# Kernel optimization log

Hardware: AMD Instinct MI355X
Metric: run time of the kernel (lower is better)

## Reference

```python
import jax, jax.numpy as jnp
import numpy as np
from jax import lax

NPOINT, RADIUS, NSAMPLE, EPS = 2048, 0.1, 32, 1e-5


def setup_inputs() -> dict:
    key = jax.random.key(0)
    ks = jax.random.split(key, 8)
    B, N, D, CIN, COUT, DEPTH = 4, 8192, 29, 32, 64, 2
    return {
        "xyz": jax.random.uniform(ks[0], (B, 3, N), jnp.float32),
        "points": jax.random.normal(ks[1], (B, D, N), jnp.float32),
        "proj_w": jax.random.normal(ks[2], (COUT, CIN), jnp.float32) * 0.05,
        "proj_g": jnp.ones((COUT,), jnp.float32),
        "proj_b": jnp.zeros((COUT,), jnp.float32),
        "w1": jax.random.normal(ks[3], (DEPTH, COUT, COUT), jnp.float32) * 0.05,
        "g1": jnp.ones((DEPTH, COUT), jnp.float32),
        "b1": jnp.zeros((DEPTH, COUT), jnp.float32),
        "w2": jax.random.normal(ks[4], (DEPTH, COUT, COUT), jnp.float32) * 0.05,
        "g2": jnp.ones((DEPTH, COUT), jnp.float32),
        "b2": jnp.zeros((DEPTH, COUT), jnp.float32),
    }


def fps(xyz, npoint):
    # xyz: [B,N,3] -> idx [B,npoint]; deterministic start at index 0
    B, N, _ = xyz.shape
    def body(carry, _):
        dist, far = carry  # [B,N], [B]
        centroid = jnp.take_along_axis(xyz, far[:, None, None], axis=1)  # [B,1,3]
        d = jnp.sum((xyz - centroid) ** 2, -1)
        dist = jnp.minimum(dist, d)
        return (dist, jnp.argmax(dist, -1).astype(jnp.int32)), far
    init = (jnp.full((B, N), 1e10, xyz.dtype), jnp.zeros((B,), jnp.int32))
    _, idx = lax.scan(body, init, None, length=npoint)
    return jnp.transpose(idx)  # [B,npoint]


def ball_query(radius, nsample, xyz, new_xyz):
    # matches torch query_ball_point: invalid -> N, sort, take first nsample, backfill
    N = xyz.shape[1]
    sqr = (jnp.sum(new_xyz ** 2, -1)[:, :, None]
           + jnp.sum(xyz ** 2, -1)[:, None, :]
           - 2.0 * jnp.einsum("bsc,bnc->bsn", new_xyz, xyz))  # [B,S,N]
    cand = jnp.where(sqr <= radius * radius, jnp.arange(N, dtype=jnp.int32), jnp.int32(N))
    neg, _ = lax.top_k(-cand, nsample)
    idx = -neg  # nsample smallest indices, ascending
    first = idx[:, :, :1]
    return jnp.where(idx == N, first, idx)  # [B,S,K]


def gather_nb(p, idx):
    # p [B,N,C], idx [B,S,K] -> [B,S,K,C]
    return jax.vmap(lambda pb, ib: pb[ib])(p, idx)


def _conv(x, w):
    # 1x1 conv: w [O,C], x [B,C,K,S]
    return jnp.einsum("oc,bcks->boks", w, x)


def _bn(x, g, b):
    # training-mode BatchNorm2d over (B,K,S) per channel
    m = jnp.mean(x, (0, 2, 3), keepdims=True)
    v = jnp.var(x, (0, 2, 3), keepdims=True)
    return g[None, :, None, None] * (x - m) * lax.rsqrt(v + EPS) + b[None, :, None, None]


def reference(xyz, points, proj_w, proj_g, proj_b, w1, g1, b1, w2, g2, b2):
    xyz_t = jnp.transpose(xyz, (0, 2, 1))      # [B,N,3]
    pts_t = jnp.transpose(points, (0, 2, 1))   # [B,N,D]
    fidx = fps(xyz_t, NPOINT)                  # [B,S]
    new_xyz = jnp.take_along_axis(xyz_t, fidx[:, :, None], axis=1)  # [B,S,3]
    idx = ball_query(RADIUS, NSAMPLE, xyz_t, new_xyz)               # [B,S,K]
    grouped_xyz = gather_nb(xyz_t, idx) - new_xyz[:, :, None, :]    # [B,S,K,3]
    grouped_pts = gather_nb(pts_t, idx)                             # [B,S,K,D]
    new_points = jnp.concatenate([grouped_xyz, grouped_pts], -1)    # [B,S,K,3+D]
    x = jnp.transpose(new_points, (0, 3, 2, 1))                     # [B,C,K,S]
    x = jax.nn.relu(_bn(_conv(x, proj_w), proj_g, proj_b))
    for d in range(w1.shape[0]):
        idn = x
        x = jax.nn.relu(_bn(_conv(x, w1[d]), g1[d], b1[d]))
        x = _bn(_conv(x, w2[d]), g2[d], b2[d])
        x = jax.nn.relu(x + idn)
    feat = jnp.max(x, axis=2)                  # [B,Cout,S]
    return jnp.transpose(new_xyz, (0, 2, 1)), feat
```

## Files before the change

### kernel.cpp

```cpp
#include <hip/hip_runtime.h>
#include <cstdint>
#include <cstddef>

#define NPTS    8192
#define NPT     2048
#define KNB     32
#define NB      4
#define DPTS    29
#define CINP    32
#define CO      64
#define KS      (KNB*NPT)
#define TELEM   ((size_t)NB*CO*KS)
#define MCNT    262144.0f
#define BNEPS   1e-5f
#define FTHR    1024
#define FWAVES  (FTHR/64)
#define FPT     8

typedef float v2f __attribute__((ext_vector_type(2)));

#define FPS_PAIR(P, A, B)                                                     \
    {                                                                         \
        v2f dx_, dy_, dz_, xx_, yy_, zz_, ss_, dd_;                           \
        asm("v_pk_add_f32 %0, %1, %2" : "=v"(dx_) : "v"(px##P), "v"(ncx));    \
        asm("v_pk_add_f32 %0, %1, %2" : "=v"(dy_) : "v"(py##P), "v"(ncy));    \
        asm("v_pk_add_f32 %0, %1, %2" : "=v"(dz_) : "v"(pz##P), "v"(ncz));    \
        asm("v_pk_mul_f32 %0, %1, %1" : "=v"(xx_) : "v"(dx_));                \
        asm("v_pk_mul_f32 %0, %1, %1" : "=v"(yy_) : "v"(dy_));                \
        asm("v_pk_mul_f32 %0, %1, %1" : "=v"(zz_) : "v"(dz_));                \
        asm("v_pk_add_f32 %0, %1, %2" : "=v"(ss_) : "v"(xx_), "v"(yy_));      \
        asm("v_pk_add_f32 %0, %1, %2" : "=v"(dd_) : "v"(ss_), "v"(zz_));      \
        float ndA = fminf(d##A, dd_.x);  d##A = ndA;                          \
        float ndB = fminf(d##B, dd_.y);  d##B = ndB;                          \
        tb = fmaxf(fmaxf(tb, ndA), ndB);                                      \
    }

static __device__ __forceinline__ unsigned long long umax64(unsigned long long a,
                                                            unsigned long long b) {
    return a > b ? a : b;
}

__global__ __launch_bounds__(FTHR) void fps_kernel(const float* __restrict__ xyz,
                                                   float* __restrict__ out0) {
    const int b = blockIdx.x;
    const int t = threadIdx.x;
    const int lane = t & 63;
    const int wid  = t >> 6;
    const float* xb = xyz + (size_t)b * 3 * NPTS;
    const int base = t * FPT;

    extern __shared__ float smem[];
    float* sx = smem;
    float* sy = sx + NPTS;
    float* sz = sy + NPTS;
    float* sc = sz + NPTS;
    unsigned long long* skey = (unsigned long long*)(sc + 3 * NPT);

    v2f px0,px1,px2,px3;
    v2f py0,py1,py2,py3;
    v2f pz0,pz1,pz2,pz3;
    float d0,d1,d2,d3,d4,d5,d6,d7;
    {
        const float4* x4 = (const float4*)(xb + base);
        const float4* y4 = (const float4*)(xb + NPTS + base);
        const float4* z4 = (const float4*)(xb + 2 * NPTS + base);
        float4* lx4 = (float4*)(sx + base);
        float4* ly4 = (float4*)(sy + base);
        float4* lz4 = (float4*)(sz + base);
        float4 v;
        v = x4[0]; lx4[0] = v; px0 = (v2f){v.x, v.y}; px1 = (v2f){v.z, v.w};
        v = x4[1]; lx4[1] = v; px2 = (v2f){v.x, v.y}; px3 = (v2f){v.z, v.w};
        v = y4[0]; ly4[0] = v; py0 = (v2f){v.x, v.y}; py1 = (v2f){v.z, v.w};
        v = y4[1]; ly4[1] = v; py2 = (v2f){v.x, v.y}; py3 = (v2f){v.z, v.w};
        v = z4[0]; lz4[0] = v; pz0 = (v2f){v.x, v.y}; pz1 = (v2f){v.z, v.w};
        v = z4[1]; lz4[1] = v; pz2 = (v2f){v.x, v.y}; pz3 = (v2f){v.z, v.w};
        d0=d1=d2=d3=d4=d5=d6=d7 = 1e10f;
    }

    float cx = xb[0], cy = xb[NPTS], cz = xb[2 * NPTS];
    float* ob = out0 + (size_t)b * 3 * NPT;
    if (t == 0) { sc[0] = cx; sc[NPT] = cy; sc[2 * NPT] = cz; }

    for (int i = 1; i < NPT; ++i) {
        const v2f ncx = (v2f){-cx, -cx};
        const v2f ncy = (v2f){-cy, -cy};
        const v2f ncz = (v2f){-cz, -cz};
        float tb = -1.0f;
        FPS_PAIR(0, 0, 1)   FPS_PAIR(1, 2, 3)
        FPS_PAIR(2, 4, 5)   FPS_PAIR(3, 6, 7)

        int jj = 0;
        jj = (d7 == tb) ? 7 : jj;
        jj = (d6 == tb) ? 6 : jj;
        jj = (d5 == tb) ? 5 : jj;
        jj = (d4 == tb) ? 4 : jj;
        jj = (d3 == tb) ? 3 : jj;
        jj = (d2 == tb) ? 2 : jj;
        jj = (d1 == tb) ? 1 : jj;
        jj = (d0 == tb) ? 0 : jj;
        const int gidx = base + jj;

        float r = tb;
        asm volatile(
            "s_nop 1\n\t"
            "v_max_f32 %0, %0, %0 row_shr:1\n\t"
            "s_nop 1\n\t"
            "v_max_f32 %0, %0, %0 row_shr:2\n\t"
            "s_nop 1\n\t"
            "v_max_f32 %0, %0, %0 row_shr:4\n\t"
            "s_nop 1\n\t"
            "v_max_f32 %0, %0, %0 row_shr:8\n\t"
            "s_nop 1\n\t"
            "v_max_f32 %0, %0, %0 row_bcast:15 row_mask:0xa\n\t"
            "s_nop 1\n\t"
            "v_max_f32 %0, %0, %0 row_bcast:31 row_mask:0xc\n\t"
            "s_nop 1"
            : "+v"(r));
        const float wm = __uint_as_float(
            (unsigned int)__builtin_amdgcn_readlane((int)__float_as_uint(r), 63));

        unsigned long long eq = __ballot(tb == wm);
        const int lwin = __ffsll((long long)eq) - 1;
        const int wgid = __builtin_amdgcn_readlane(gidx, lwin);

        const int par = i & 1;
        if (lane == 0)
            skey[par * FWAVES + wid] =
                (((unsigned long long)__float_as_uint(wm)) << 32) |
                (unsigned int)(~(unsigned int)wgid);
        __syncthreads();

        const ulonglong2* sk2 = (const ulonglong2*)(skey + par * FWAVES);
        ulonglong2 k01 = sk2[0], k23 = sk2[1], k45 = sk2[2], k67 = sk2[3];
        ulonglong2 k89 = sk2[4], kab = sk2[5], kcd = sk2[6], kef = sk2[7];
        unsigned long long ka = umax64(umax64(k01.x, k01.y), umax64(k23.x, k23.y));
        unsigned long long kb = umax64(umax64(k45.x, k45.y), umax64(k67.x, k67.y));
        unsigned long long kc = umax64(umax64(k89.x, k89.y), umax64(kab.x, kab.y));
        unsigned long long kd = umax64(umax64(kcd.x, kcd.y), umax64(kef.x, kef.y));
        unsigned long long kbest = umax64(umax64(ka, kb), umax64(kc, kd));
        const int widx = (int)(~(unsigned int)kbest);

        cx = sx[widx]; cy = sy[widx]; cz = sz[widx];
        if (t == 0) { sc[i] = cx; sc[NPT + i] = cy; sc[2 * NPT + i] = cz; }
    }

    __syncthreads();
    const float4* s4 = (const float4*)sc;
    float4* o4 = (float4*)ob;
    for (int e = t; e < 3 * NPT / 4; e += FTHR) o4[e] = s4[e];
}

__global__ __launch_bounds__(256) void ballq_kernel(const float* __restrict__ xyz,
                                                    const float* __restrict__ out0,
                                                    int* __restrict__ idx) {
    const int gw   = (blockIdx.x * 256 + threadIdx.x) >> 6;
    const int lane = threadIdx.x & 63;
    const int b  = gw >> 11;
    const int si = gw & 2047;
    const float* xb = xyz + (size_t)b * 3 * NPTS;

    const float cx = out0[b * 3 * NPT + si];
    const float cy = out0[b * 3 * NPT + NPT + si];
    const float cz = out0[b * 3 * NPT + 2*NPT + si];
    const float csum = __fadd_rn(__fadd_rn(__fmul_rn(cx, cx), __fmul_rn(cy, cy)),
                                 __fmul_rn(cz, cz));
    const float R2 = (float)(0.1 * 0.1);

    __shared__ int buf[4][KNB];
    int* mybuf = buf[threadIdx.x >> 6];

    int cnt = 0;
    for (int n0 = 0; n0 < NPTS && cnt < KNB; n0 += 64) {
        const int i = n0 + lane;
        float pxv = xb[i], pyv = xb[NPTS + i], pzv = xb[2 * NPTS + i];
        float ps = __fadd_rn(__fadd_rn(__fmul_rn(pxv, pxv), __fmul_rn(pyv, pyv)),
                             __fmul_rn(pzv, pzv));
        float dot = __fmaf_rn(pzv, cz, __fmaf_rn(pyv, cy, __fmul_rn(pxv, cx)));
        float sqr = __fsub_rn(__fadd_rn(csum, ps), __fadd_rn(dot, dot));
        bool hit = (sqr <= R2);
        unsigned long long m = __ballot(hit);
        int pos = cnt + __popcll(m & ((1ull << lane) - 1ull));
        if (hit && pos < KNB) mybuf[pos] = i;
        cnt += __popcll(m);
    }
    int c = cnt < KNB ? cnt : KNB;
    int first = (cnt > 0) ? mybuf[0] : 0;
    if (lane < KNB) {
        int v = (lane < c) ? mybuf[lane] : first;
        idx[((size_t)gw << 5) + lane] = v;
    }
}

__global__ __launch_bounds__(256) void proj_kernel(const float* __restrict__ xyz,
                                                   const float* __restrict__ points,
                                                   const float* __restrict__ out0,
                                                   const int* __restrict__ idx,
                                                   const float* __restrict__ W,
                                                   float* __restrict__ out,
                                                   float* __restrict__ stats) {
    const int p = blockIdx.x * 256 + threadIdx.x;
    const int b = p >> 16;
    const int q = p & 65535;
    const int k = q >> 11;
    const int s = q & 2047;
    const int tid = threadIdx.x;

    __shared__ float ssum[CO], ssq[CO];
    if (tid < CO) { ssum[tid] = 0.f; ssq[tid] = 0.f; }
    __syncthreads();

    const int j = idx[((size_t)(b * NPT + s) << 5) + k];
    const float* xb = xyz + (size_t)b * 3 * NPTS;
    float a[CINP];
    a[0] = xb[j]            - out0[b * 3 * NPT + s];
    a[1] = xb[NPTS + j]     - out0[b * 3 * NPT + NPT + s];
    a[2] = xb[2*NPTS + j]   - out0[b * 3 * NPT + 2*NPT + s];
    const float* pb = points + (size_t)b * DPTS * NPTS;
#pragma unroll
    for (int c = 0; c < DPTS; ++c) a[3 + c] = pb[c * NPTS + j];

    const size_t obase = (size_t)b * CO * KS + q;
    for (int o = 0; o < CO; ++o) {
        float acc = 0.f;
#pragma unroll
        for (int c = 0; c < CINP; ++c) acc = __fmaf_rn(W[o * CINP + c], a[c], acc);
        out[obase + (size_t)o * KS] = acc;
        float s1 = acc, s2 = acc * acc;
#pragma unroll
        for (int off = 32; off > 0; off >>= 1) {
            s1 += __shfl_xor(s1, off, 64);
            s2 += __shfl_xor(s2, off, 64);
        }
        if ((tid & 63) == 0) { atomicAdd(&ssum[o], s1); atomicAdd(&ssq[o], s2); }
    }
    __syncthreads();
    if (tid < CO) {
        atomicAdd(&stats[tid], ssum[tid]);
        atomicAdd(&stats[CO + tid], ssq[tid]);
    }
}

template <bool HAS_IDN, bool WRITE_ACT>
__global__ __launch_bounds__(256) void conv_bn_kernel(const float* in,
                                                      const float* idn,
                                                      const float* __restrict__ stats_in,
                                                      const float* __restrict__ gamma,
                                                      const float* __restrict__ beta,
                                                      const float* __restrict__ W,
                                                      float* act_out,
                                                      float* out,
                                                      float* __restrict__ stats_out) {
    const int p = blockIdx.x * 256 + threadIdx.x;
    const int b = p >> 16;
    const int q = p & 65535;
    const int tid = threadIdx.x;

    __shared__ float ssc[CO], ssh[CO], ssum[CO], ssq[CO];
    if (tid < CO) {
        const float Minv = 1.0f / MCNT;
        float m = stats_in[tid] * Minv;
        float v = stats_in[CO + tid] * Minv - m * m;
        float scl = gamma[tid] * rsqrtf(v + BNEPS);
        ssc[tid] = scl;
        ssh[tid] = beta[tid] - m * scl;
        ssum[tid] = 0.f; ssq[tid] = 0.f;
    }
    __syncthreads();

    const size_t base = (size_t)b * CO * KS + q;
    float a[CO];
#pragma unroll
    for (int c = 0; c < CO; ++c) {
        float v = __fmaf_rn(ssc[c], in[base + (size_t)c * KS], ssh[c]);
        if (HAS_IDN) v += idn[base + (size_t)c * KS];
        v = fmaxf(v, 0.0f);
        a[c] = v;
        if (WRITE_ACT) act_out[base + (size_t)c * KS] = v;
    }
    for (int o = 0; o < CO; ++o) {
        float acc = 0.f;
#pragma unroll
        for (int c = 0; c < CO; ++c) acc = __fmaf_rn(W[o * CO + c], a[c], acc);
        out[base + (size_t)o * KS] = acc;
        float s1 = acc, s2 = acc * acc;
#pragma unroll
        for (int off = 32; off > 0; off >>= 1) {
            s1 += __shfl_xor(s1, off, 64);
            s2 += __shfl_xor(s2, off, 64);
        }
        if ((tid & 63) == 0) { atomicAdd(&ssum[o], s1); atomicAdd(&ssq[o], s2); }
    }
    __syncthreads();
    if (tid < CO) {
        atomicAdd(&stats_out[tid], ssum[tid]);
        atomicAdd(&stats_out[CO + tid], ssq[tid]);
    }
}

__global__ __launch_bounds__(256) void final_kernel(const float* __restrict__ y2,
                                                    const float* __restrict__ idn,
                                                    const float* __restrict__ stats,
                                                    const float* __restrict__ gamma,
                                                    const float* __restrict__ beta,
                                                    float* __restrict__ feat) {
    const int p = blockIdx.x * 256 + threadIdx.x;
    const int s = p & 2047;
    const int o = (p >> 11) & 63;
    const int b = p >> 17;
    const float Minv = 1.0f / MCNT;
    float m = stats[o] * Minv;
    float v = stats[CO + o] * Minv - m * m;
    float scl = gamma[o] * rsqrtf(v + BNEPS);
    float sh  = beta[o] - m * scl;
    const size_t base = (size_t)b * CO * KS + (size_t)o * KS + s;
    float mx = -1e30f;
#pragma unroll
    for (int k = 0; k < KNB; ++k) {
        float val = __fmaf_rn(scl, y2[base + (size_t)k * NPT], sh) + idn[base + (size_t)k * NPT];
        val = fmaxf(val, 0.0f);
        mx = fmaxf(mx, val);
    }
    feat[p] = mx;
}

__global__ void zero_kernel(float* p, int n) {
    int i = blockIdx.x * blockDim.x + threadIdx.x;
    if (i < n) p[i] = 0.f;
}

extern "C" void kernel_launch(void* const* d_in, const int* in_sizes, int n_in,
                              void* d_out, int out_size, void* d_ws, size_t ws_size,
                              hipStream_t stream) {
    (void)in_sizes; (void)n_in; (void)out_size; (void)ws_size;
    const float* xyz    = (const float*)d_in[0];
    const float* points = (const float*)d_in[1];
    const float* proj_w = (const float*)d_in[2];
    const float* proj_g = (const float*)d_in[3];
    const float* proj_b = (const float*)d_in[4];
    const float* w1     = (const float*)d_in[5];
    const float* g1     = (const float*)d_in[6];
    const float* b1     = (const float*)d_in[7];
    const float* w2     = (const float*)d_in[8];
    const float* g2     = (const float*)d_in[9];
    const float* b2     = (const float*)d_in[10];

    float* out0 = (float*)d_out;
    float* feat = (float*)d_out + NB * 3 * NPT;

    float* stats = (float*)d_ws;
    int*   idx   = (int*)((float*)d_ws + 1024);
    float* A     = (float*)(idx + NB * NPT * KNB);
    float* B     = A + TELEM;

    const size_t fps_lds = (size_t)(3 * NPTS + 3 * NPT) * sizeof(float)
                         + 2 * FWAVES * sizeof(unsigned long long);

    hipLaunchKernelGGL(zero_kernel, dim3(3), dim3(256), 0, stream, stats, 5 * 2 * CO);
    hipLaunchKernelGGL(fps_kernel, dim3(NB), dim3(FTHR), fps_lds, stream, xyz, out0);
    hipLaunchKernelGGL(ballq_kernel, dim3(2048), dim3(256), 0, stream, xyz, out0, idx);
    hipLaunchKernelGGL(proj_kernel, dim3(1024), dim3(256), 0, stream,
                       xyz, points, out0, idx, proj_w, A, stats);
    hipLaunchKernelGGL((conv_bn_kernel<false, true>), dim3(1024), dim3(256), 0, stream,
                       A, (const float*)nullptr, stats, proj_g, proj_b, w1,
                       B, A, stats + 128);
    hipLaunchKernelGGL((conv_bn_kernel<false, false>), dim3(1024), dim3(256), 0, stream,
                       A, (const float*)nullptr, stats + 128, g1, b1, w2,
                       (float*)nullptr, A, stats + 256);
    hipLaunchKernelGGL((conv_bn_kernel<true, true>), dim3(1024), dim3(256), 0, stream,
                       A, B, stats + 256, g2, b2, w1 + CO * CO,
                       B, A, stats + 384);
    hipLaunchKernelGGL((conv_bn_kernel<false, false>), dim3(1024), dim3(256), 0, stream,
                       A, (const float*)nullptr, stats + 384, g1 + CO, b1 + CO, w2 + CO * CO,
                       (float*)nullptr, A, stats + 512);
    hipLaunchKernelGGL(final_kernel, dim3(2048), dim3(256), 0, stream,
                       A, B, stats + 512, g2 + CO, b2 + CO, feat);
}
```

Measured before the change: 2.892 ms.

## Shrink FPS block to 256 threads with 32 points per thread

The FPS kernel now runs 256 threads per block, each holding 32 points in registers instead of 8. The per-thread argmax becomes a tree reduction, and the cross-wave shared-memory reduction reads 4 wave keys instead of 16. The aim is to cut per-iteration barrier and cross-wave reduction cost in the 2048-step serial loop, in exchange for more per-thread serial work and higher register pressure. The hand-written packed-math asm is replaced by vector-typed C code, with fp contraction disabled to keep the rounding bit-exact.

```diff
diff --git a/kernel.cpp b/kernel.cpp
--- a/kernel.cpp
+++ b/kernel.cpp
@@ -1,6 +1,8 @@
 #include <hip/hip_runtime.h>
 #include <cstdint>
 #include <cstddef>
+
+#pragma clang fp contract(off)
 
 #define NPTS    8192
 #define NPT     2048
@@ -13,27 +15,11 @@
 #define TELEM   ((size_t)NB*CO*KS)
 #define MCNT    262144.0f
 #define BNEPS   1e-5f
-#define FTHR    1024
+#define FTHR    256
 #define FWAVES  (FTHR/64)
-#define FPT     8
+#define FPT     32
 
 typedef float v2f __attribute__((ext_vector_type(2)));
-
-#define FPS_PAIR(P, A, B)                                                     \
-    {                                                                         \
-        v2f dx_, dy_, dz_, xx_, yy_, zz_, ss_, dd_;                           \
-        asm("v_pk_add_f32 %0, %1, %2" : "=v"(dx_) : "v"(px##P), "v"(ncx));    \
-        asm("v_pk_add_f32 %0, %1, %2" : "=v"(dy_) : "v"(py##P), "v"(ncy));    \
-        asm("v_pk_add_f32 %0, %1, %2" : "=v"(dz_) : "v"(pz##P), "v"(ncz));    \
-        asm("v_pk_mul_f32 %0, %1, %1" : "=v"(xx_) : "v"(dx_));                \
-        asm("v_pk_mul_f32 %0, %1, %1" : "=v"(yy_) : "v"(dy_));                \
-        asm("v_pk_mul_f32 %0, %1, %1" : "=v"(zz_) : "v"(dz_));                \
-        asm("v_pk_add_f32 %0, %1, %2" : "=v"(ss_) : "v"(xx_), "v"(yy_));      \
-        asm("v_pk_add_f32 %0, %1, %2" : "=v"(dd_) : "v"(ss_), "v"(zz_));      \
-        float ndA = fminf(d##A, dd_.x);  d##A = ndA;                          \
-        float ndB = fminf(d##B, dd_.y);  d##B = ndB;                          \
-        tb = fmaxf(fmaxf(tb, ndA), ndB);                                      \
-    }
 
 static __device__ __forceinline__ unsigned long long umax64(unsigned long long a,
                                                             unsigned long long b) {
@@ -56,10 +42,8 @@
     float* sc = sz + NPTS;
     unsigned long long* skey = (unsigned long long*)(sc + 3 * NPT);
 
-    v2f px0,px1,px2,px3;
-    v2f py0,py1,py2,py3;
-    v2f pz0,pz1,pz2,pz3;
-    float d0,d1,d2,d3,d4,d5,d6,d7;
+    v2f px[16], py[16], pz[16];
+    float d[32];
     {
         const float4* x4 = (const float4*)(xb + base);
         const float4* y4 = (const float4*)(xb + NPTS + base);
@@ -67,14 +51,15 @@
         float4* lx4 = (float4*)(sx + base);
         float4* ly4 = (float4*)(sy + base);
         float4* lz4 = (float4*)(sz + base);
-        float4 v;
-        v = x4[0]; lx4[0] = v; px0 = (v2f){v.x, v.y}; px1 = (v2f){v.z, v.w};
-        v = x4[1]; lx4[1] = v; px2 = (v2f){v.x, v.y}; px3 = (v2f){v.z, v.w};
-        v = y4[0]; ly4[0] = v; py0 = (v2f){v.x, v.y}; py1 = (v2f){v.z, v.w};
-        v = y4[1]; ly4[1] = v; py2 = (v2f){v.x, v.y}; py3 = (v2f){v.z, v.w};
-        v = z4[0]; lz4[0] = v; pz0 = (v2f){v.x, v.y}; pz1 = (v2f){v.z, v.w};
-        v = z4[1]; lz4[1] = v; pz2 = (v2f){v.x, v.y}; pz3 = (v2f){v.z, v.w};
-        d0=d1=d2=d3=d4=d5=d6=d7 = 1e10f;
+#pragma unroll
+        for (int u = 0; u < 8; ++u) {
+            float4 v;
+            v = x4[u]; lx4[u] = v; px[2*u] = (v2f){v.x, v.y}; px[2*u+1] = (v2f){v.z, v.w};
+            v = y4[u]; ly4[u] = v; py[2*u] = (v2f){v.x, v.y}; py[2*u+1] = (v2f){v.z, v.w};
+            v = z4[u]; lz4[u] = v; pz[2*u] = (v2f){v.x, v.y}; pz[2*u+1] = (v2f){v.z, v.w};
+        }
+#pragma unroll
+        for (int k = 0; k < 32; ++k) d[k] = 1e10f;
     }
 
     float cx = xb[0], cy = xb[NPTS], cz = xb[2 * NPTS];
@@ -85,19 +70,42 @@
         const v2f ncx = (v2f){-cx, -cx};
         const v2f ncy = (v2f){-cy, -cy};
         const v2f ncz = (v2f){-cz, -cz};
-        float tb = -1.0f;
-        FPS_PAIR(0, 0, 1)   FPS_PAIR(1, 2, 3)
-        FPS_PAIR(2, 4, 5)   FPS_PAIR(3, 6, 7)
-
-        int jj = 0;
-        jj = (d7 == tb) ? 7 : jj;
-        jj = (d6 == tb) ? 6 : jj;
-        jj = (d5 == tb) ? 5 : jj;
-        jj = (d4 == tb) ? 4 : jj;
-        jj = (d3 == tb) ? 3 : jj;
-        jj = (d2 == tb) ? 2 : jj;
-        jj = (d1 == tb) ? 1 : jj;
-        jj = (d0 == tb) ? 0 : jj;
+#pragma unroll
+        for (int p = 0; p < 16; ++p) {
+            v2f dx = px[p] + ncx;
+            v2f dy = py[p] + ncy;
+            v2f dz = pz[p] + ncz;
+            v2f dd = (dx * dx + dy * dy) + dz * dz;
+            d[2*p]   = fminf(d[2*p],   dd.x);
+            d[2*p+1] = fminf(d[2*p+1], dd.y);
+        }
+
+        float v16[16]; int j16[16];
+#pragma unroll
+        for (int k = 0; k < 16; ++k) {
+            v16[k] = fmaxf(d[2*k], d[2*k+1]);
+            j16[k] = (d[2*k] >= d[2*k+1]) ? 2*k : 2*k+1;
+        }
+        float v8[8]; int j8[8];
+#pragma unroll
+        for (int k = 0; k < 8; ++k) {
+            v8[k] = fmaxf(v16[2*k], v16[2*k+1]);
+            j8[k] = (v16[2*k] >= v16[2*k+1]) ? j16[2*k] : j16[2*k+1];
+        }
+        float v4[4]; int j4[4];
+#pragma unroll
+        for (int k = 0; k < 4; ++k) {
+            v4[k] = fmaxf(v8[2*k], v8[2*k+1]);
+            j4[k] = (v8[2*k] >= v8[2*k+1]) ? j8[2*k] : j8[2*k+1];
+        }
+        float v2[2]; int j2[2];
+#pragma unroll
+        for (int k = 0; k < 2; ++k) {
+            v2[k] = fmaxf(v4[2*k], v4[2*k+1]);
+            j2[k] = (v4[2*k] >= v4[2*k+1]) ? j4[2*k] : j4[2*k+1];
+        }
+        const float tb = fmaxf(v2[0], v2[1]);
+        const int   jj = (v2[0] >= v2[1]) ? j2[0] : j2[1];
         const int gidx = base + jj;
 
         float r = tb;
@@ -131,13 +139,9 @@
         __syncthreads();
 
         const ulonglong2* sk2 = (const ulonglong2*)(skey + par * FWAVES);
-        ulonglong2 k01 = sk2[0], k23 = sk2[1], k45 = sk2[2], k67 = sk2[3];
-        ulonglong2 k89 = sk2[4], kab = sk2[5], kcd = sk2[6], kef = sk2[7];
-        unsigned long long ka = umax64(umax64(k01.x, k01.y), umax64(k23.x, k23.y));
-        unsigned long long kb = umax64(umax64(k45.x, k45.y), umax64(k67.x, k67.y));
-        unsigned long long kc = umax64(umax64(k89.x, k89.y), umax64(kab.x, kab.y));
-        unsigned long long kd = umax64(umax64(kcd.x, kcd.y), umax64(kef.x, kef.y));
-        unsigned long long kbest = umax64(umax64(ka, kb), umax64(kc, kd));
+        ulonglong2 k01 = sk2[0], k23 = sk2[1];
+        unsigned long long kbest = umax64(umax64(k01.x, k01.y),
+                                          umax64(k23.x, k23.y));
         const int widx = (int)(~(unsigned int)kbest);
 
         cx = sx[widx]; cy = sy[widx]; cz = sz[widx];
@@ -147,6 +151,7 @@
     __syncthreads();
     const float4* s4 = (const float4*)sc;
     float4* o4 = (float4*)ob;
+#pragma unroll
     for (int e = t; e < 3 * NPT / 4; e += FTHR) o4[e] = s4[e];
 }
 
```

Result: slower. 3.917 ms (+35.4%).
